# Performance work log

Hardware: AMD Instinct MI355X
Metric: run time of the kernel (lower is better)

The kernel has to match this reference:

```python
import jax, jax.numpy as jnp
import numpy as np
from jax.scipy.linalg import expm as _expm

B, D = 1024, 128
_SQRT3 = 3.0 ** 0.5
_C1, _C2 = 0.5 - _SQRT3 / 6.0, 0.5 + _SQRT3 / 6.0


def setup_inputs() -> dict:
    key = jax.random.key(0)
    k_t, k_y, k_a, k_w = jax.random.split(key, 4)
    scale = 1.0 / np.sqrt(D)  # keep ||Omega|| moderate so expm is well-conditioned
    return {
        "t0": jax.random.uniform(k_t, (B,), dtype=jnp.float32),
        "h": jnp.float32(0.1),
        "y0": jax.random.normal(k_y, (B, D), dtype=jnp.float32),
        "A0": jax.random.normal(k_a, (B, D, D), dtype=jnp.float32) * scale,
        "W": jax.random.normal(k_w, (B, D, D), dtype=jnp.float32) * scale,
    }


def reference(t0, h, y0, A0, W):
    # A(t) = A0 + t * W evaluated at the two Gauss-Legendre nodes
    t1 = t0 + _C1 * h  # (B,)
    t2 = t0 + _C2 * h  # (B,)
    A1 = A0 + t1[:, None, None] * W  # (B, D, D)
    A2 = A0 + t2[:, None, None] * W  # (B, D, D)
    alpha1 = (h * 0.5) * (A1 + A2)
    alpha2 = (h * _SQRT3) * (A2 - A1)
    comm = alpha1 @ alpha2 - alpha2 @ alpha1  # [alpha1, alpha2]
    Omega = alpha1 - comm / 12.0
    U = jax.vmap(_expm)(Omega)  # batched matrix exponential (B, D, D)
    y_next = jnp.einsum("bij,bj->bi", U, y0)  # (B, D)
    return y_next, jnp.stack((A1, A2), axis=0)
```

## Files before the change

kernel.cpp:

```cpp
#include <hip/hip_runtime.h>

#define B_SZ 1024
#define D_SZ 128
#define KTERMS 7
#define QPAD 36

typedef float vfloat4 __attribute__((ext_vector_type(4)));

__device__ inline float bflo(unsigned u) { return __uint_as_float(u << 16); }
__device__ inline float bfhi(unsigned u) { return __uint_as_float(u & 0xffff0000u); }

__device__ inline float dot32(const unsigned* rq, const float* v) {
    float a0 = 0.f, a1 = 0.f, a2 = 0.f, a3 = 0.f;
#pragma unroll
    for (int j = 0; j < 8; ++j) {
        vfloat4 vv = *(const vfloat4*)(v + 4 * j);
        a0 = fmaf(bflo(rq[2 * j]),     vv.x, a0);
        a1 = fmaf(bfhi(rq[2 * j]),     vv.y, a1);
        a2 = fmaf(bflo(rq[2 * j + 1]), vv.z, a2);
        a3 = fmaf(bfhi(rq[2 * j + 1]), vv.w, a3);
    }
    return (a0 + a1) + (a2 + a3);
}

__global__ void __launch_bounds__(512, 4)
magnus_kernel(const float* __restrict__ t0p, const float* __restrict__ hp,
              const float* __restrict__ y0, const float* __restrict__ A0,
              const float* __restrict__ W, float* __restrict__ out)
{
    __shared__ __align__(16) float svr [4 * QPAD];
    __shared__ __align__(16) float su1r[4 * QPAD];
    __shared__ __align__(16) float su2r[4 * QPAD];
    __shared__ __align__(16) float su3r[4 * QPAD];
    __shared__ __align__(16) float su4r[4 * QPAD];

    const int tid   = threadIdx.x;
    const int grpid = blockIdx.x >> 3;
    const int job   = grpid & 1;
    const int b     = ((grpid >> 1) << 3) + (blockIdx.x & 7);

    const float h  = hp[0];
    const float tb = t0p[b];
    const size_t moff = (size_t)b * (D_SZ * D_SZ);

    if (job == 0) {
        const float SQ3_6 = 0.28867513459481287f;
        const float t1 = tb + (0.5f - SQ3_6) * h;
        const float t2 = tb + (0.5f + SQ3_6) * h;
        const float4* A0v = (const float4*)(A0 + moff);
        const float4* Wv  = (const float4*)(W + moff);
        vfloat4* o1 = (vfloat4*)(out + (size_t)B_SZ * D_SZ + moff);
        vfloat4* o2 = (vfloat4*)(out + (size_t)B_SZ * D_SZ
                                     + (size_t)B_SZ * D_SZ * D_SZ + moff);
#pragma unroll 8
        for (int it = 0; it < 8; ++it) {
            int i = it * 512 + tid;
            float4 a = A0v[i];
            float4 w = Wv[i];
            vfloat4 p1, p2;
            p1.x = fmaf(t1, w.x, a.x); p1.y = fmaf(t1, w.y, a.y);
            p1.z = fmaf(t1, w.z, a.z); p1.w = fmaf(t1, w.w, a.w);
            p2.x = fmaf(t2, w.x, a.x); p2.y = fmaf(t2, w.y, a.y);
            p2.z = fmaf(t2, w.z, a.z); p2.w = fmaf(t2, w.w, a.w);
            __builtin_nontemporal_store(p1, o1 + i);
            __builtin_nontemporal_store(p2, o2 + i);
        }
        return;
    }

    const int row = tid >> 2;
    const int q   = tid & 3;
    const int fbase = row * 32 + q * 8;

    const float4* Ap = (const float4*)(A0 + moff) + fbase;
    const float4* Wp = (const float4*)(W + moff) + fbase;
    unsigned ra[16], rw[16];
#pragma unroll
    for (int it = 0; it < 8; ++it) {
        float4 a = Ap[it];
        float4 w = Wp[it];
        asm("v_cvt_pk_bf16_f32 %0, %1, %2" : "=v"(ra[2*it])   : "v"(a.x), "v"(a.y));
        asm("v_cvt_pk_bf16_f32 %0, %1, %2" : "=v"(ra[2*it+1]) : "v"(a.z), "v"(a.w));
        asm("v_cvt_pk_bf16_f32 %0, %1, %2" : "=v"(rw[2*it])   : "v"(w.x), "v"(w.y));
        asm("v_cvt_pk_bf16_f32 %0, %1, %2" : "=v"(rw[2*it+1]) : "v"(w.z), "v"(w.w));
    }

    float yacc = 0.0f;
    if (tid < D_SZ) {
        float v = y0[(size_t)b * D_SZ + tid];
        svr[(tid >> 5) * QPAD + (tid & 31)] = v;
        yacc = v;
    }
    __syncthreads();

    const float hs = h * (tb + 0.5f * h);
    const float c3 = h * h * h * (1.0f / 12.0f);
    const int uflat = (row >> 5) * QPAD + (row & 31);

#pragma unroll
    for (int k = 1; k <= KTERMS; ++k) {
        {
            const float* vq = svr + q * QPAD;
            float pa = dot32(ra, vq);
            float pw = dot32(rw, vq);
            pa += __shfl_xor(pa, 1); pa += __shfl_xor(pa, 2);
            pw += __shfl_xor(pw, 1); pw += __shfl_xor(pw, 2);
            if (q == 0) { su1r[uflat] = pa; su2r[uflat] = pw; }
        }
        __syncthreads();
        {
            float pb = dot32(ra, su2r + q * QPAD);
            float pc = dot32(rw, su1r + q * QPAD);
            pb += __shfl_xor(pb, 1); pb += __shfl_xor(pb, 2);
            pc += __shfl_xor(pc, 1); pc += __shfl_xor(pc, 2);
            if (q == 0) { su3r[uflat] = pb; su4r[uflat] = pc; }
        }
        __syncthreads();
        if (tid < D_SZ) {
            int f = (tid >> 5) * QPAD + (tid & 31);
            float wn = h * su1r[f] + hs * su2r[f] - c3 * (su3r[f] - su4r[f]);
            wn *= (1.0f / (float)k);
            yacc += wn;
            svr[f] = wn;
        }
        __syncthreads();
    }

    if (tid < D_SZ) {
        out[(size_t)b * D_SZ + tid] = yacc;
    }
}

extern "C" void kernel_launch(void* const* d_in, const int* in_sizes, int n_in,
                              void* d_out, int out_size, void* d_ws, size_t ws_size,
                              hipStream_t stream) {
    const float* t0 = (const float*)d_in[0];
    const float* h  = (const float*)d_in[1];
    const float* y0 = (const float*)d_in[2];
    const float* A0 = (const float*)d_in[3];
    const float* W  = (const float*)d_in[4];
    float* out = (float*)d_out;
    magnus_kernel<<<2 * B_SZ, 512, 0, stream>>>(t0, h, y0, A0, W, out);
}
```

Before: 252.2 us.

## Fuse A1/A2 writer blocks with Taylor-series blocks and cut per-iteration barriers

Replaces the split grid of 2*B blocks with B blocks. Each block now both writes A1/A2 and runs the Taylor-series matrix-vector iterations, so the A0 and W tiles are fetched by one block instead of two separate ones. The iteration loop also fuses the A and W dot products into a single pass over the vector. The combining step is done in registers by every lane, which removes two shared buffers and one barrier per term. The cost is higher register pressure from holding fp32 tiles across the store loop under the existing launch bounds, plus losing the overlap between independent writer and compute blocks.

Result: slower. 264.5 us (+4.8%).

```diff
diff --git a/kernel.cpp b/kernel.cpp
--- a/kernel.cpp
+++ b/kernel.cpp
@@ -10,15 +10,34 @@
 __device__ inline float bflo(unsigned u) { return __uint_as_float(u << 16); }
 __device__ inline float bfhi(unsigned u) { return __uint_as_float(u & 0xffff0000u); }
 
-__device__ inline float dot32(const unsigned* rq, const float* v) {
-    float a0 = 0.f, a1 = 0.f, a2 = 0.f, a3 = 0.f;
+__device__ inline void dot32x2(const unsigned* ra, const unsigned* rw,
+                               const float* v, float& oa, float& ow) {
+    float a0=0.f,a1=0.f,a2=0.f,a3=0.f, w0=0.f,w1=0.f,w2=0.f,w3=0.f;
 #pragma unroll
     for (int j = 0; j < 8; ++j) {
         vfloat4 vv = *(const vfloat4*)(v + 4 * j);
-        a0 = fmaf(bflo(rq[2 * j]),     vv.x, a0);
-        a1 = fmaf(bfhi(rq[2 * j]),     vv.y, a1);
-        a2 = fmaf(bflo(rq[2 * j + 1]), vv.z, a2);
-        a3 = fmaf(bfhi(rq[2 * j + 1]), vv.w, a3);
+        a0 = fmaf(bflo(ra[2*j]),   vv.x, a0);
+        a1 = fmaf(bfhi(ra[2*j]),   vv.y, a1);
+        a2 = fmaf(bflo(ra[2*j+1]), vv.z, a2);
+        a3 = fmaf(bfhi(ra[2*j+1]), vv.w, a3);
+        w0 = fmaf(bflo(rw[2*j]),   vv.x, w0);
+        w1 = fmaf(bfhi(rw[2*j]),   vv.y, w1);
+        w2 = fmaf(bflo(rw[2*j+1]), vv.z, w2);
+        w3 = fmaf(bfhi(rw[2*j+1]), vv.w, w3);
+    }
+    oa = (a0 + a1) + (a2 + a3);
+    ow = (w0 + w1) + (w2 + w3);
+}
+
+__device__ inline float dot32(const unsigned* rq, const float* v) {
+    float a0=0.f,a1=0.f,a2=0.f,a3=0.f;
+#pragma unroll
+    for (int j = 0; j < 8; ++j) {
+        vfloat4 vv = *(const vfloat4*)(v + 4 * j);
+        a0 = fmaf(bflo(rq[2*j]),   vv.x, a0);
+        a1 = fmaf(bfhi(rq[2*j]),   vv.y, a1);
+        a2 = fmaf(bflo(rq[2*j+1]), vv.z, a2);
+        a3 = fmaf(bfhi(rq[2*j+1]), vv.w, a3);
     }
     return (a0 + a1) + (a2 + a3);
 }
@@ -31,22 +50,28 @@
     __shared__ __align__(16) float svr [4 * QPAD];
     __shared__ __align__(16) float su1r[4 * QPAD];
     __shared__ __align__(16) float su2r[4 * QPAD];
-    __shared__ __align__(16) float su3r[4 * QPAD];
-    __shared__ __align__(16) float su4r[4 * QPAD];
 
-    const int tid   = threadIdx.x;
-    const int grpid = blockIdx.x >> 3;
-    const int job   = grpid & 1;
-    const int b     = ((grpid >> 1) << 3) + (blockIdx.x & 7);
-
+    const int b   = blockIdx.x;
+    const int tid = threadIdx.x;
+    const int row = tid >> 2;
+    const int q   = tid & 3;
     const float h  = hp[0];
     const float tb = t0p[b];
+    const float SQ3_6 = 0.28867513459481287f;
+    const float t1 = tb + (0.5f - SQ3_6) * h;
+    const float t2 = tb + (0.5f + SQ3_6) * h;
+
     const size_t moff = (size_t)b * (D_SZ * D_SZ);
 
-    if (job == 0) {
-        const float SQ3_6 = 0.28867513459481287f;
-        const float t1 = tb + (0.5f - SQ3_6) * h;
-        const float t2 = tb + (0.5f + SQ3_6) * h;
+    const int fbase = row * 32 + q * 8;
+    const float4* Ap = (const float4*)(A0 + moff) + fbase;
+    const float4* Wp = (const float4*)(W + moff) + fbase;
+    float4 ta[8], tw[8];
+#pragma unroll
+    for (int it = 0; it < 8; ++it) { ta[it] = Ap[it]; tw[it] = Wp[it]; }
+    float yv = y0[(size_t)b * D_SZ + row];
+
+    {
         const float4* A0v = (const float4*)(A0 + moff);
         const float4* Wv  = (const float4*)(W + moff);
         vfloat4* o1 = (vfloat4*)(out + (size_t)B_SZ * D_SZ + moff);
@@ -65,31 +90,20 @@
             __builtin_nontemporal_store(p1, o1 + i);
             __builtin_nontemporal_store(p2, o2 + i);
         }
-        return;
     }
 
-    const int row = tid >> 2;
-    const int q   = tid & 3;
-    const int fbase = row * 32 + q * 8;
-
-    const float4* Ap = (const float4*)(A0 + moff) + fbase;
-    const float4* Wp = (const float4*)(W + moff) + fbase;
     unsigned ra[16], rw[16];
 #pragma unroll
     for (int it = 0; it < 8; ++it) {
-        float4 a = Ap[it];
-        float4 w = Wp[it];
-        asm("v_cvt_pk_bf16_f32 %0, %1, %2" : "=v"(ra[2*it])   : "v"(a.x), "v"(a.y));
-        asm("v_cvt_pk_bf16_f32 %0, %1, %2" : "=v"(ra[2*it+1]) : "v"(a.z), "v"(a.w));
-        asm("v_cvt_pk_bf16_f32 %0, %1, %2" : "=v"(rw[2*it])   : "v"(w.x), "v"(w.y));
-        asm("v_cvt_pk_bf16_f32 %0, %1, %2" : "=v"(rw[2*it+1]) : "v"(w.z), "v"(w.w));
+        asm("v_cvt_pk_bf16_f32 %0, %1, %2" : "=v"(ra[2*it])   : "v"(ta[it].x), "v"(ta[it].y));
+        asm("v_cvt_pk_bf16_f32 %0, %1, %2" : "=v"(ra[2*it+1]) : "v"(ta[it].z), "v"(ta[it].w));
+        asm("v_cvt_pk_bf16_f32 %0, %1, %2" : "=v"(rw[2*it])   : "v"(tw[it].x), "v"(tw[it].y));
+        asm("v_cvt_pk_bf16_f32 %0, %1, %2" : "=v"(rw[2*it+1]) : "v"(tw[it].z), "v"(tw[it].w));
     }
 
-    float yacc = 0.0f;
+    float yacc = yv;
     if (tid < D_SZ) {
-        float v = y0[(size_t)b * D_SZ + tid];
-        svr[(tid >> 5) * QPAD + (tid & 31)] = v;
-        yacc = v;
+        svr[(tid >> 5) * QPAD + (tid & 31)] = y0[(size_t)b * D_SZ + tid];
     }
     __syncthreads();
 
@@ -99,35 +113,26 @@
 
 #pragma unroll
     for (int k = 1; k <= KTERMS; ++k) {
-        {
-            const float* vq = svr + q * QPAD;
-            float pa = dot32(ra, vq);
-            float pw = dot32(rw, vq);
-            pa += __shfl_xor(pa, 1); pa += __shfl_xor(pa, 2);
-            pw += __shfl_xor(pw, 1); pw += __shfl_xor(pw, 2);
-            if (q == 0) { su1r[uflat] = pa; su2r[uflat] = pw; }
+        float pa, pw;
+        dot32x2(ra, rw, svr + q * QPAD, pa, pw);
+        pa += __shfl_xor(pa, 1); pa += __shfl_xor(pa, 2);
+        pw += __shfl_xor(pw, 1); pw += __shfl_xor(pw, 2);
+        if (q == 0) { su1r[uflat] = pa; su2r[uflat] = pw; }
+        __syncthreads();
+        float pb = dot32(ra, su2r + q * QPAD);
+        float pc = dot32(rw, su1r + q * QPAD);
+        pb += __shfl_xor(pb, 1); pb += __shfl_xor(pb, 2);
+        pc += __shfl_xor(pc, 1); pc += __shfl_xor(pc, 2);
+        float wn = (h * pa + hs * pw - c3 * (pb - pc)) * (1.0f / (float)k);
+        yacc += wn;
+        if (k < KTERMS) {
+            if (q == 0) svr[uflat] = wn;
+            __syncthreads();
         }
-        __syncthreads();
-        {
-            float pb = dot32(ra, su2r + q * QPAD);
-            float pc = dot32(rw, su1r + q * QPAD);
-            pb += __shfl_xor(pb, 1); pb += __shfl_xor(pb, 2);
-            pc += __shfl_xor(pc, 1); pc += __shfl_xor(pc, 2);
-            if (q == 0) { su3r[uflat] = pb; su4r[uflat] = pc; }
-        }
-        __syncthreads();
-        if (tid < D_SZ) {
-            int f = (tid >> 5) * QPAD + (tid & 31);
-            float wn = h * su1r[f] + hs * su2r[f] - c3 * (su3r[f] - su4r[f]);
-            wn *= (1.0f / (float)k);
-            yacc += wn;
-            svr[f] = wn;
-        }
-        __syncthreads();
     }
 
-    if (tid < D_SZ) {
-        out[(size_t)b * D_SZ + tid] = yacc;
+    if (q == 0) {
+        out[(size_t)b * D_SZ + row] = yacc;
     }
 }
 
@@ -140,5 +145,5 @@
     const float* A0 = (const float*)d_in[3];
     const float* W  = (const float*)d_in[4];
     float* out = (float*)d_out;
-    magnus_kernel<<<2 * B_SZ, 512, 0, stream>>>(t0, h, y0, A0, W, out);
+    magnus_kernel<<<B_SZ, 512, 0, stream>>>(t0, h, y0, A0, W, out);
 }
```
